# Kernel optimization log

Measured on AMD Instinct MI355X. Metric: run time of the kernel, lower is better.

## Reference

```python
import math
import jax, jax.numpy as jnp
import numpy as np

NQ = 10      # n_qubits
NB = 4       # n_blocks (angle encoding layers)
VD = 6       # vqc_depth (hardware-efficient layers)
LAT = 128    # latent_dim
NOBS = 9     # n_qubits - k_local + 1 sliding 2-local groups
DIM = 2 ** NQ


def sin_embed(t, dim):
    half = dim // 2
    freqs = jnp.exp(-math.log(10000.0) * jnp.arange(half, dtype=jnp.float32) / half)
    args = t[:, None] * freqs[None, :]
    return jnp.concatenate([jnp.cos(args), jnp.sin(args)], axis=-1)


def apply_ry(psi, theta, q):
    # psi: [B, 2^NQ] complex; theta: scalar or [B]
    B = psi.shape[0]
    p = psi.reshape(B, 2 ** q, 2, 2 ** (NQ - 1 - q))
    th = jnp.broadcast_to(theta, (B,))
    c = jnp.cos(th / 2)[:, None, None].astype(psi.dtype)
    s = jnp.sin(th / 2)[:, None, None].astype(psi.dtype)
    p0, p1 = p[:, :, 0, :], p[:, :, 1, :]
    return jnp.stack([c * p0 - s * p1, s * p0 + c * p1], axis=2).reshape(B, -1)


def apply_cnot(psi, ctrl, tgt):
    B = psi.shape[0]
    pt = psi.reshape((B,) + (2,) * NQ)
    p0 = jax.lax.index_in_dim(pt, 0, axis=ctrl + 1, keepdims=True)
    p1 = jnp.flip(jax.lax.index_in_dim(pt, 1, axis=ctrl + 1, keepdims=True), axis=tgt + 1)
    return jnp.concatenate([p0, p1], axis=ctrl + 1).reshape(B, -1)


def run_circuit(enc, var_params):
    B = enc.shape[0]
    psi = jnp.zeros((B, DIM), dtype=jnp.complex64).at[:, 0].set(1.0)
    # angle encoding: RY data re-uploading blocks with CNOT ladders between blocks
    for layer in range(NB):
        for q in range(NQ):
            psi = apply_ry(psi, enc[:, layer * NQ + q], q)
        if layer < NB - 1:
            for q in range(0, NQ - 1, 2):
                psi = apply_cnot(psi, q, q + 1)
            for q in range(1, NQ - 1, 2):
                psi = apply_cnot(psi, q, q + 1)
    # hardware-efficient variational layers
    for ly in range(VD):
        for q in range(NQ):
            psi = apply_ry(psi, var_params[ly, q], q)
        for q in range(0, NQ - 1, 2):
            psi = apply_cnot(psi, q, q + 1)
        for q in range(1, NQ - 1, 2):
            psi = apply_cnot(psi, q, q + 1)
    return psi


def build_H(A_p, B_p, D_p):
    # create_Hermitian: lower-tri (row-major) = A + iB; h[i-1,i-1] = D[i]; H = h + h^dagger
    r, c = np.tril_indices(4, -1)  # order matches count+j loop: (1,0),(2,0),(2,1),(3,0),(3,1),(3,2)
    L = jnp.zeros((NOBS, 4, 4), dtype=jnp.complex64)
    L = L.at[:, r, c].set(A_p.astype(jnp.complex64) + 1j * B_p.astype(jnp.complex64))
    d = 2.0 * jnp.concatenate([D_p[:, 1:4], jnp.zeros((NOBS, 1), dtype=D_p.dtype)], axis=1)
    H = L + jnp.conj(jnp.swapaxes(L, 1, 2))
    H = H + jax.vmap(jnp.diag)(d).astype(jnp.complex64)
    return H


def expvals(psi, H):
    B = psi.shape[0]
    outs = []
    for s in range(NOBS):  # sliding window [s, s+1]
        pg = psi.reshape(B, 2 ** s, 4, 2 ** (NQ - s - 2))
        outs.append(jnp.einsum('balr,lk,bakr->b', jnp.conj(pg), H[s], pg).real)
    return jnp.stack(outs, axis=-1)


def setup_inputs() -> dict:
    ks = jax.random.split(jax.random.key(0), 12)
    B = 2048
    return {
        'z_t': jax.random.normal(ks[0], (B, LAT), dtype=jnp.float32),
        't': jax.random.uniform(ks[1], (B,), dtype=jnp.float32),
        'W1': 0.05 * jax.random.normal(ks[2], (2 * LAT, 256), dtype=jnp.float32),
        'b1': jnp.zeros((256,), dtype=jnp.float32),
        'W2': 0.05 * jax.random.normal(ks[3], (256, NB * NQ), dtype=jnp.float32),
        'b2': jnp.zeros((NB * NQ,), dtype=jnp.float32),
        'var_params': 0.01 * jax.random.normal(ks[4], (VD, NQ), dtype=jnp.float32),
        'A_p': 2.0 * jax.random.normal(ks[5], (NOBS, 6), dtype=jnp.float32),
        'B_p': 2.0 * jax.random.normal(ks[6], (NOBS, 6), dtype=jnp.float32),
        'D_p': 2.0 * jax.random.normal(ks[7], (NOBS, 4), dtype=jnp.float32),
        'W3': 0.05 * jax.random.normal(ks[8], (NOBS, 256), dtype=jnp.float32),
        'b3': jnp.zeros((256,), dtype=jnp.float32),
        'W4': 0.05 * jax.random.normal(ks[9], (256, LAT), dtype=jnp.float32),
        'b4': jnp.zeros((LAT,), dtype=jnp.float32),
    }


def reference(z_t, t, W1, b1, W2, b2, var_params, A_p, B_p, D_p, W3, b3, W4, b4):
    x = jnp.concatenate([z_t, sin_embed(t, LAT)], axis=-1)   # [B, 2*LAT]
    h = jax.nn.silu(x @ W1 + b1)
    enc = h @ W2 + b2                                         # [B, NB*NQ]
    psi = run_circuit(enc, var_params)                        # [B, 2^NQ]
    obs = expvals(psi, build_H(A_p, B_p, D_p))                # [B, NOBS]
    return jax.nn.silu(obs @ W3 + b3) @ W4 + b4               # [B, LAT]
```

## Files before the change

### kernel.cpp

```cpp
#include <hip/hip_runtime.h>
#include <math.h>

#define NOBS 9
#define LATD 128

typedef unsigned u32x2 __attribute__((ext_vector_type(2)));

__device__ __forceinline__ float silu_f(float x) { return x / (1.f + expf(-x)); }


template<int CTRL>
__device__ __forceinline__ float dpp_perm(float x) {
  return __int_as_float(__builtin_amdgcn_update_dpp(0, __float_as_int(x), CTRL, 0xF, 0xF, true));
}
template<int PAT>
__device__ __forceinline__ float ds_swz(float x) {
  return __int_as_float(__builtin_amdgcn_ds_swizzle(__float_as_int(x), PAT));
}

__device__ __forceinline__ float x4(float x) { return ds_swz<0x101F>(x); }

#if __has_builtin(__builtin_amdgcn_permlane32_swap)
#define PL32 1
__device__ __forceinline__ float x32(float x, bool sel) {
  u32x2 r = __builtin_amdgcn_permlane32_swap(__float_as_uint(x), __float_as_uint(x), false, false);
  return __uint_as_float(sel ? r.x : r.y);
}
__device__ __forceinline__ float sum32(float x) {
  u32x2 r = __builtin_amdgcn_permlane32_swap(__float_as_uint(x), __float_as_uint(x), false, false);
  return __uint_as_float(r.x) + __uint_as_float(r.y);
}
#else
#define PL32 0
__device__ __forceinline__ float x32(float x, bool sel) { return __shfl_xor(x, 32, 64); }
__device__ __forceinline__ float sum32(float x) { return x + __shfl_xor(x, 32, 64); }
#endif

#if __has_builtin(__builtin_amdgcn_permlane16_swap)
#define PL16 1
__device__ __forceinline__ float x16(float x, bool sel) {
  u32x2 r = __builtin_amdgcn_permlane16_swap(__float_as_uint(x), __float_as_uint(x), false, false);
  return __uint_as_float(sel ? r.x : r.y);
}
__device__ __forceinline__ float sum16(float x) {
  u32x2 r = __builtin_amdgcn_permlane16_swap(__float_as_uint(x), __float_as_uint(x), false, false);
  return __uint_as_float(r.x) + __uint_as_float(r.y);
}
#else
#define PL16 0
__device__ __forceinline__ float x16(float x, bool sel) { return ds_swz<0x401F>(x); }
__device__ __forceinline__ float sum16(float x) { return x + ds_swz<0x401F>(x); }
#endif

__device__ __forceinline__ float wave_sum(float x) {
  x += dpp_perm<0xB1>(x);
  x += dpp_perm<0x4E>(x);
  x += x4(x);
  x += dpp_perm<0x128>(x);
  x = sum16(x);
  x = sum32(x);
  return x;
}


template<int M>
__device__ __forceinline__ void ry_reg(float v[16], float c, float s) {
#pragma unroll
  for (int r = 0; r < 16; ++r) {
    if ((r & M) == 0) {
      float p0 = v[r], p1 = v[r | M];
      v[r]     = c * p0 - s * p1;
      v[r | M] = s * p0 + c * p1;
    }
  }
}

__device__ __forceinline__ void apply_rys(float v[16], int lane, bool sel32, bool sel16,
                                          const float* __restrict__ cc,
                                          const float* __restrict__ ss) {
  ry_reg<8>(v, cc[0], ss[0]);
  ry_reg<4>(v, cc[1], ss[1]);
  ry_reg<2>(v, cc[2], ss[2]);
  ry_reg<1>(v, cc[3], ss[3]);
  { float c = cc[4], s = ss[4], sp = (lane & 32) ? s : -s;
#pragma unroll
    for (int r = 0; r < 16; ++r) { float p = x32(v[r], sel32); v[r] = fmaf(c, v[r], sp * p); } }
  { float c = cc[5], s = ss[5], sp = (lane & 16) ? s : -s;
#pragma unroll
    for (int r = 0; r < 16; ++r) { float p = x16(v[r], sel16); v[r] = fmaf(c, v[r], sp * p); } }
  { float c = cc[6], s = ss[6], sp = (lane & 8) ? s : -s;
#pragma unroll
    for (int r = 0; r < 16; ++r) { float p = dpp_perm<0x128>(v[r]); v[r] = fmaf(c, v[r], sp * p); } }
  { float c = cc[7], s = ss[7], sp = (lane & 4) ? s : -s;
#pragma unroll
    for (int r = 0; r < 16; ++r) { float p = x4(v[r]); v[r] = fmaf(c, v[r], sp * p); } }
  { float c = cc[8], s = ss[8], sp = (lane & 2) ? s : -s;
#pragma unroll
    for (int r = 0; r < 16; ++r) { float p = dpp_perm<0x4E>(v[r]); v[r] = fmaf(c, v[r], sp * p); } }
  { float c = cc[9], s = ss[9], sp = (lane & 1) ? s : -s;
#pragma unroll
    for (int r = 0; r < 16; ++r) { float p = dpp_perm<0xB1>(v[r]); v[r] = fmaf(c, v[r], sp * p); } }
}

__device__ __forceinline__ void cnot_ladder(float v[16], int lane, bool sel32, bool sel16) {
  float t;
  t=v[8];  v[8]=v[12];  v[12]=t;
  t=v[9];  v[9]=v[13];  v[13]=t;
  t=v[10]; v[10]=v[14]; v[14]=t;
  t=v[11]; v[11]=v[15]; v[15]=t;
  t=v[2];  v[2]=v[3];   v[3]=t;
  t=v[6];  v[6]=v[7];   v[7]=t;
  t=v[10]; v[10]=v[11]; v[11]=t;
  t=v[14]; v[14]=v[15]; v[15]=t;
  { bool c45 = (lane & 32);
#pragma unroll
    for (int r = 0; r < 16; ++r) { float p = x16(v[r], sel16); v[r] = c45 ? p : v[r]; } }
  { bool c67 = (lane & 8);
#pragma unroll
    for (int r = 0; r < 16; ++r) { float p = x4(v[r]); v[r] = c67 ? p : v[r]; } }
  { bool c89 = (lane & 2);
#pragma unroll
    for (int r = 0; r < 16; ++r) { float p = dpp_perm<0xB1>(v[r]); v[r] = c89 ? p : v[r]; } }
  t=v[4];  v[4]=v[6];   v[6]=t;
  t=v[5];  v[5]=v[7];   v[7]=t;
  t=v[12]; v[12]=v[14]; v[14]=t;
  t=v[13]; v[13]=v[15]; v[15]=t;
#pragma unroll
  for (int r = 1; r < 16; r += 2) v[r] = x32(v[r], sel32);
  { bool c56 = (lane & 16);
#pragma unroll
    for (int r = 0; r < 16; ++r) { float p = dpp_perm<0x128>(v[r]); v[r] = c56 ? p : v[r]; } }
  { bool c78 = (lane & 4);
#pragma unroll
    for (int r = 0; r < 16; ++r) { float p = dpp_perm<0x4E>(v[r]); v[r] = c78 ? p : v[r]; } }
}


__global__ __launch_bounds__(256) void fused_kernel(
    const float* __restrict__ z, const float* __restrict__ t,
    const float* __restrict__ W1, const float* __restrict__ b1,
    const float* __restrict__ W2, const float* __restrict__ b2,
    const float* __restrict__ varp,
    const float* __restrict__ A_p, const float* __restrict__ D_p,
    const float* __restrict__ W3, const float* __restrict__ b3,
    const float* __restrict__ W4, const float* __restrict__ b4,
    float* __restrict__ out) {
  __shared__ float xs[4][256];
  __shared__ float hs[4][256];
  __shared__ float dump[4][1024];
  __shared__ float cs[4][40], sn[4][40];
  __shared__ float vcs[60], vsn[60];
  __shared__ float os[4][NOBS];

  int tid = threadIdx.x;
  int b0 = blockIdx.x * 4;

  if (tid < 60) {
    float s, c;
    sincosf(0.5f * varp[tid], &s, &c);
    vcs[tid] = c; vsn[tid] = s;
  }

#pragma unroll
  for (int r = 0; r < 4; ++r) {
    int b = b0 + r;
    if (tid < 128) {
      xs[r][tid] = z[b * 128 + tid];
    } else {
      int i = tid - 128, j = i & 63;
      float freq = expf(-9.2103403719761836f * (float)j * (1.f / 64.f));
      float arg = t[b] * freq;
      xs[r][tid] = (i < 64) ? cosf(arg) : sinf(arg);
    }
  }
  __syncthreads();

  {
    float bv = b1[tid];
    float a0 = bv, a1 = bv, a2 = bv, a3 = bv;
#pragma unroll 4
    for (int k = 0; k < 256; k += 4) {
      float w0 = W1[(k + 0) * 256 + tid];
      float w1 = W1[(k + 1) * 256 + tid];
      float w2 = W1[(k + 2) * 256 + tid];
      float w3 = W1[(k + 3) * 256 + tid];
      float4 x0 = *(const float4*)&xs[0][k];
      float4 x1 = *(const float4*)&xs[1][k];
      float4 x2 = *(const float4*)&xs[2][k];
      float4 x3 = *(const float4*)&xs[3][k];
      a0 = fmaf(x0.w, w3, fmaf(x0.z, w2, fmaf(x0.y, w1, fmaf(x0.x, w0, a0))));
      a1 = fmaf(x1.w, w3, fmaf(x1.z, w2, fmaf(x1.y, w1, fmaf(x1.x, w0, a1))));
      a2 = fmaf(x2.w, w3, fmaf(x2.z, w2, fmaf(x2.y, w1, fmaf(x2.x, w0, a2))));
      a3 = fmaf(x3.w, w3, fmaf(x3.z, w2, fmaf(x3.y, w1, fmaf(x3.x, w0, a3))));
    }
    hs[0][tid] = silu_f(a0);
    hs[1][tid] = silu_f(a1);
    hs[2][tid] = silu_f(a2);
    hs[3][tid] = silu_f(a3);
  }
  __syncthreads();

  if (tid < 160) {
    int r = tid / 40, c = tid - r * 40;
    float acc = b2[c];
#pragma unroll 4
    for (int k = 0; k < 256; k += 4) {
      float4 h = *(const float4*)&hs[r][k];
      acc = fmaf(h.x, W2[(k + 0) * 40 + c], acc);
      acc = fmaf(h.y, W2[(k + 1) * 40 + c], acc);
      acc = fmaf(h.z, W2[(k + 2) * 40 + c], acc);
      acc = fmaf(h.w, W2[(k + 3) * 40 + c], acc);
    }
    float s, cv;
    sincosf(0.5f * acc, &s, &cv);
    cs[r][c] = cv; sn[r][c] = s;
  }
  __syncthreads();

  {
    int wave = tid >> 6;
    int lane = tid & 63;
    bool sel32 = true, sel16 = true;
#if PL32
    { u32x2 tt = __builtin_amdgcn_permlane32_swap((unsigned)lane, (unsigned)lane, false, false);
      sel32 = (tt.x == (unsigned)(lane ^ 32)); }
#endif
#if PL16
    { u32x2 tt = __builtin_amdgcn_permlane16_swap((unsigned)lane, (unsigned)lane, false, false);
      sel16 = (tt.x == (unsigned)(lane ^ 16)); }
#endif
    const float* cc = cs[wave];
    const float* ss = sn[wave];

    float base = 1.f;
    base *= (lane & 32) ? ss[4] : cc[4];
    base *= (lane & 16) ? ss[5] : cc[5];
    base *= (lane & 8)  ? ss[6] : cc[6];
    base *= (lane & 4)  ? ss[7] : cc[7];
    base *= (lane & 2)  ? ss[8] : cc[8];
    base *= (lane & 1)  ? ss[9] : cc[9];
    float v[16];
#pragma unroll
    for (int r = 0; r < 16; ++r) {
      float p = base;
      p *= (r & 8) ? ss[0] : cc[0];
      p *= (r & 4) ? ss[1] : cc[1];
      p *= (r & 2) ? ss[2] : cc[2];
      p *= (r & 1) ? ss[3] : cc[3];
      v[r] = p;
    }
    cnot_ladder(v, lane, sel32, sel16);
#pragma unroll 1
    for (int layer = 1; layer < 4; ++layer) {
      apply_rys(v, lane, sel32, sel16, cc + layer * 10, ss + layer * 10);
      if (layer < 3) cnot_ladder(v, lane, sel32, sel16);
    }
#pragma unroll 1
    for (int ly = 0; ly < 6; ++ly) {
      apply_rys(v, lane, sel32, sel16, vcs + ly * 10, vsn + ly * 10);
      cnot_ladder(v, lane, sel32, sel16);
    }

    float* sw = dump[wave];
#pragma unroll
    for (int r = 0; r < 16; ++r) sw[r * 64 + lane] = v[r];

#pragma unroll 1
    for (int s = 0; s < NOBS; ++s) {
      const int r8 = 8 - s;
      const int stride = 1 << r8;
      float h10 = A_p[s*6+0], h20 = A_p[s*6+1], h21 = A_p[s*6+2];
      float h30 = A_p[s*6+3], h31 = A_p[s*6+4], h32 = A_p[s*6+5];
      float d0 = 2.f * D_p[s*4+1], d1 = 2.f * D_p[s*4+2], d2 = 2.f * D_p[s*4+3];
      float acc = 0.f;
#pragma unroll
      for (int k = 0; k < 4; ++k) {
        int p = lane + 64 * k;
        int a  = p >> r8;
        int rr = p & (stride - 1);
        int bse = (a << (r8 + 2)) + rr;
        float x0 = sw[bse];
        float x1 = sw[bse + stride];
        float x2 = sw[bse + 2 * stride];
        float x3 = sw[bse + 3 * stride];
        acc += d0 * x0 * x0 + d1 * x1 * x1 + d2 * x2 * x2
             + 2.f * (h10 * x1 * x0 + h20 * x2 * x0 + h21 * x2 * x1
                    + h30 * x3 * x0 + h31 * x3 * x1 + h32 * x3 * x2);
      }
      acc = wave_sum(acc);
      if (lane == 0) os[wave][s] = acc;
    }
  }
  __syncthreads();

  {
    float bv = b3[tid];
    float a0 = bv, a1 = bv, a2 = bv, a3 = bv;
#pragma unroll
    for (int s = 0; s < NOBS; ++s) {
      float w = W3[s * 256 + tid];
      a0 = fmaf(os[0][s], w, a0);
      a1 = fmaf(os[1][s], w, a1);
      a2 = fmaf(os[2][s], w, a2);
      a3 = fmaf(os[3][s], w, a3);
    }
    hs[0][tid] = silu_f(a0);
    hs[1][tid] = silu_f(a1);
    hs[2][tid] = silu_f(a2);
    hs[3][tid] = silu_f(a3);
  }
  __syncthreads();
  {
    int c = tid & 127, rg = tid >> 7;
    const float* h0 = hs[rg * 2];
    const float* h1 = hs[rg * 2 + 1];
    float o0 = b4[c], o1 = b4[c];
#pragma unroll 4
    for (int k = 0; k < 256; k += 4) {
      float w0 = W4[(k + 0) * 128 + c];
      float w1 = W4[(k + 1) * 128 + c];
      float w2 = W4[(k + 2) * 128 + c];
      float w3 = W4[(k + 3) * 128 + c];
      float4 ha = *(const float4*)&h0[k];
      float4 hb = *(const float4*)&h1[k];
      o0 = fmaf(ha.w, w3, fmaf(ha.z, w2, fmaf(ha.y, w1, fmaf(ha.x, w0, o0))));
      o1 = fmaf(hb.w, w3, fmaf(hb.z, w2, fmaf(hb.y, w1, fmaf(hb.x, w0, o1))));
    }
    out[(b0 + rg * 2) * LATD + c]     = o0;
    out[(b0 + rg * 2 + 1) * LATD + c] = o1;
  }
}


extern "C" void kernel_launch(void* const* d_in, const int* in_sizes, int n_in,
                              void* d_out, int out_size, void* d_ws, size_t ws_size,
                              hipStream_t stream) {
  const float* z_t  = (const float*)d_in[0];
  const float* t    = (const float*)d_in[1];
  const float* W1   = (const float*)d_in[2];
  const float* b1   = (const float*)d_in[3];
  const float* W2   = (const float*)d_in[4];
  const float* b2   = (const float*)d_in[5];
  const float* varp = (const float*)d_in[6];
  const float* A_p  = (const float*)d_in[7];
  const float* D_p  = (const float*)d_in[9];
  const float* W3   = (const float*)d_in[10];
  const float* b3   = (const float*)d_in[11];
  const float* W4   = (const float*)d_in[12];
  const float* b4   = (const float*)d_in[13];
  float* out = (float*)d_out;

  int B = in_sizes[1];

  fused_kernel<<<B / 4, 256, 0, stream>>>(z_t, t, W1, b1, W2, b2, varp,
                                          A_p, D_p, W3, b3, W4, b4, out);
}
```

Baseline: 128.8 us.

## Split each statevector across two waves with LDS exchange for top qubit

Each batch row's 1024-amplitude state is now split across two wavefronts (8 registers each instead of 16), with the most significant qubit's RY handled by exchanging halves through shared memory under a block barrier. Blocks now process 2 rows instead of 4, doubling the grid, and the permlane swap intrinsics are replaced with plain shfl_xor. The intent is more parallelism and lower register pressure per wave. The cost is a __syncthreads per RY layer, double the W1/W4 weight traffic per row, and slower shuffle-based cross-lane ops.

Measured after the change: 128.2 us. Within noise of the previous version (-0.5%).

```diff
diff --git a/kernel.cpp b/kernel.cpp
--- a/kernel.cpp
+++ b/kernel.cpp
@@ -3,8 +3,6 @@
 
 #define NOBS 9
 #define LATD 128
-
-typedef unsigned u32x2 __attribute__((ext_vector_type(2)));
 
 __device__ __forceinline__ float silu_f(float x) { return x / (1.f + expf(-x)); }
 
@@ -17,56 +15,23 @@
 __device__ __forceinline__ float ds_swz(float x) {
   return __int_as_float(__builtin_amdgcn_ds_swizzle(__float_as_int(x), PAT));
 }
-
-__device__ __forceinline__ float x4(float x) { return ds_swz<0x101F>(x); }
-
-#if __has_builtin(__builtin_amdgcn_permlane32_swap)
-#define PL32 1
-__device__ __forceinline__ float x32(float x, bool sel) {
-  u32x2 r = __builtin_amdgcn_permlane32_swap(__float_as_uint(x), __float_as_uint(x), false, false);
-  return __uint_as_float(sel ? r.x : r.y);
-}
-__device__ __forceinline__ float sum32(float x) {
-  u32x2 r = __builtin_amdgcn_permlane32_swap(__float_as_uint(x), __float_as_uint(x), false, false);
-  return __uint_as_float(r.x) + __uint_as_float(r.y);
-}
-#else
-#define PL32 0
-__device__ __forceinline__ float x32(float x, bool sel) { return __shfl_xor(x, 32, 64); }
-__device__ __forceinline__ float sum32(float x) { return x + __shfl_xor(x, 32, 64); }
-#endif
-
-#if __has_builtin(__builtin_amdgcn_permlane16_swap)
-#define PL16 1
-__device__ __forceinline__ float x16(float x, bool sel) {
-  u32x2 r = __builtin_amdgcn_permlane16_swap(__float_as_uint(x), __float_as_uint(x), false, false);
-  return __uint_as_float(sel ? r.x : r.y);
-}
-__device__ __forceinline__ float sum16(float x) {
-  u32x2 r = __builtin_amdgcn_permlane16_swap(__float_as_uint(x), __float_as_uint(x), false, false);
-  return __uint_as_float(r.x) + __uint_as_float(r.y);
-}
-#else
-#define PL16 0
-__device__ __forceinline__ float x16(float x, bool sel) { return ds_swz<0x401F>(x); }
-__device__ __forceinline__ float sum16(float x) { return x + ds_swz<0x401F>(x); }
-#endif
+__device__ __forceinline__ float x4f(float x) { return ds_swz<0x101F>(x); }
 
 __device__ __forceinline__ float wave_sum(float x) {
   x += dpp_perm<0xB1>(x);
   x += dpp_perm<0x4E>(x);
-  x += x4(x);
+  x += x4f(x);
   x += dpp_perm<0x128>(x);
-  x = sum16(x);
-  x = sum32(x);
+  x += ds_swz<0x401F>(x);
+  x += __shfl_xor(x, 32, 64);
   return x;
 }
 
 
 template<int M>
-__device__ __forceinline__ void ry_reg(float v[16], float c, float s) {
-#pragma unroll
-  for (int r = 0; r < 16; ++r) {
+__device__ __forceinline__ void ry_reg8(float v[8], float c, float s) {
+#pragma unroll
+  for (int r = 0; r < 8; ++r) {
     if ((r & M) == 0) {
       float p0 = v[r], p1 = v[r | M];
       v[r]     = c * p0 - s * p1;
@@ -74,65 +39,78 @@
     }
   }
 }
-
-__device__ __forceinline__ void apply_rys(float v[16], int lane, bool sel32, bool sel16,
-                                          const float* __restrict__ cc,
-                                          const float* __restrict__ ss) {
-  ry_reg<8>(v, cc[0], ss[0]);
-  ry_reg<4>(v, cc[1], ss[1]);
-  ry_reg<2>(v, cc[2], ss[2]);
-  ry_reg<1>(v, cc[3], ss[3]);
-  { float c = cc[4], s = ss[4], sp = (lane & 32) ? s : -s;
-#pragma unroll
-    for (int r = 0; r < 16; ++r) { float p = x32(v[r], sel32); v[r] = fmaf(c, v[r], sp * p); } }
-  { float c = cc[5], s = ss[5], sp = (lane & 16) ? s : -s;
-#pragma unroll
-    for (int r = 0; r < 16; ++r) { float p = x16(v[r], sel16); v[r] = fmaf(c, v[r], sp * p); } }
-  { float c = cc[6], s = ss[6], sp = (lane & 8) ? s : -s;
-#pragma unroll
-    for (int r = 0; r < 16; ++r) { float p = dpp_perm<0x128>(v[r]); v[r] = fmaf(c, v[r], sp * p); } }
-  { float c = cc[7], s = ss[7], sp = (lane & 4) ? s : -s;
-#pragma unroll
-    for (int r = 0; r < 16; ++r) { float p = x4(v[r]); v[r] = fmaf(c, v[r], sp * p); } }
-  { float c = cc[8], s = ss[8], sp = (lane & 2) ? s : -s;
-#pragma unroll
-    for (int r = 0; r < 16; ++r) { float p = dpp_perm<0x4E>(v[r]); v[r] = fmaf(c, v[r], sp * p); } }
-  { float c = cc[9], s = ss[9], sp = (lane & 1) ? s : -s;
-#pragma unroll
-    for (int r = 0; r < 16; ++r) { float p = dpp_perm<0xB1>(v[r]); v[r] = fmaf(c, v[r], sp * p); } }
-}
-
-__device__ __forceinline__ void cnot_ladder(float v[16], int lane, bool sel32, bool sel16) {
-  float t;
-  t=v[8];  v[8]=v[12];  v[12]=t;
-  t=v[9];  v[9]=v[13];  v[13]=t;
-  t=v[10]; v[10]=v[14]; v[14]=t;
-  t=v[11]; v[11]=v[15]; v[15]=t;
-  t=v[2];  v[2]=v[3];   v[3]=t;
-  t=v[6];  v[6]=v[7];   v[7]=t;
-  t=v[10]; v[10]=v[11]; v[11]=t;
-  t=v[14]; v[14]=v[15]; v[15]=t;
+template<int MASK>
+__device__ __forceinline__ void ry_shfl8(float v[8], float c, float s, int lane) {
+  float sp = (lane & MASK) ? s : -s;
+#pragma unroll
+  for (int r = 0; r < 8; ++r) { float p = __shfl_xor(v[r], MASK, 64); v[r] = fmaf(c, v[r], sp * p); }
+}
+template<int CTRL, int MASK>
+__device__ __forceinline__ void ry_dpp8(float v[8], float c, float s, int lane) {
+  float sp = (lane & MASK) ? s : -s;
+#pragma unroll
+  for (int r = 0; r < 8; ++r) { float p = dpp_perm<CTRL>(v[r]); v[r] = fmaf(c, v[r], sp * p); }
+}
+__device__ __forceinline__ void ry_x4g(float v[8], float c, float s, int lane) {
+  float sp = (lane & 4) ? s : -s;
+#pragma unroll
+  for (int r = 0; r < 8; ++r) { float p = x4f(v[r]); v[r] = fmaf(c, v[r], sp * p); }
+}
+
+__device__ __forceinline__ void apply_rys10(float v[8], int lane, int w,
+                                            const float* __restrict__ cc,
+                                            const float* __restrict__ ss,
+                                            float* xbuf) {
+  {
+    float c = cc[0], s = ss[0];
+    float sp = w ? s : -s;
+    float* mine   = xbuf + w * 512;
+    float* theirs = xbuf + (1 - w) * 512;
+#pragma unroll
+    for (int r = 0; r < 8; ++r) mine[r * 64 + lane] = v[r];
+    __syncthreads();
+#pragma unroll
+    for (int r = 0; r < 8; ++r) { float p = theirs[r * 64 + lane]; v[r] = fmaf(c, v[r], sp * p); }
+  }
+  ry_reg8<4>(v, cc[1], ss[1]);
+  ry_reg8<2>(v, cc[2], ss[2]);
+  ry_reg8<1>(v, cc[3], ss[3]);
+  ry_shfl8<32>(v, cc[4], ss[4], lane);
+  ry_shfl8<16>(v, cc[5], ss[5], lane);
+  ry_dpp8<0x128, 8>(v, cc[6], ss[6], lane);
+  ry_x4g(v, cc[7], ss[7], lane);
+  ry_dpp8<0x4E, 2>(v, cc[8], ss[8], lane);
+  ry_dpp8<0xB1, 1>(v, cc[9], ss[9], lane);
+}
+
+__device__ __forceinline__ void cnot_ladder8(float v[8], int lane, int w) {
+#pragma unroll
+  for (int r = 0; r < 4; ++r) {
+    float a = v[r], b = v[r + 4];
+    v[r]     = w ? b : a;
+    v[r + 4] = w ? a : b;
+  }
+  { float t = v[2]; v[2] = v[3]; v[3] = t; }
+  { float t = v[6]; v[6] = v[7]; v[7] = t; }
   { bool c45 = (lane & 32);
 #pragma unroll
-    for (int r = 0; r < 16; ++r) { float p = x16(v[r], sel16); v[r] = c45 ? p : v[r]; } }
+    for (int r = 0; r < 8; ++r) { float p = __shfl_xor(v[r], 16, 64); v[r] = c45 ? p : v[r]; } }
   { bool c67 = (lane & 8);
 #pragma unroll
-    for (int r = 0; r < 16; ++r) { float p = x4(v[r]); v[r] = c67 ? p : v[r]; } }
+    for (int r = 0; r < 8; ++r) { float p = x4f(v[r]); v[r] = c67 ? p : v[r]; } }
   { bool c89 = (lane & 2);
 #pragma unroll
-    for (int r = 0; r < 16; ++r) { float p = dpp_perm<0xB1>(v[r]); v[r] = c89 ? p : v[r]; } }
-  t=v[4];  v[4]=v[6];   v[6]=t;
-  t=v[5];  v[5]=v[7];   v[7]=t;
-  t=v[12]; v[12]=v[14]; v[14]=t;
-  t=v[13]; v[13]=v[15]; v[15]=t;
-#pragma unroll
-  for (int r = 1; r < 16; r += 2) v[r] = x32(v[r], sel32);
+    for (int r = 0; r < 8; ++r) { float p = dpp_perm<0xB1>(v[r]); v[r] = c89 ? p : v[r]; } }
+  { float t = v[4]; v[4] = v[6]; v[6] = t; }
+  { float t = v[5]; v[5] = v[7]; v[7] = t; }
+#pragma unroll
+  for (int r = 1; r < 8; r += 2) v[r] = __shfl_xor(v[r], 32, 64);
   { bool c56 = (lane & 16);
 #pragma unroll
-    for (int r = 0; r < 16; ++r) { float p = dpp_perm<0x128>(v[r]); v[r] = c56 ? p : v[r]; } }
+    for (int r = 0; r < 8; ++r) { float p = dpp_perm<0x128>(v[r]); v[r] = c56 ? p : v[r]; } }
   { bool c78 = (lane & 4);
 #pragma unroll
-    for (int r = 0; r < 16; ++r) { float p = dpp_perm<0x4E>(v[r]); v[r] = c78 ? p : v[r]; } }
+    for (int r = 0; r < 8; ++r) { float p = dpp_perm<0x4E>(v[r]); v[r] = c78 ? p : v[r]; } }
 }
 
 
@@ -145,15 +123,16 @@
     const float* __restrict__ W3, const float* __restrict__ b3,
     const float* __restrict__ W4, const float* __restrict__ b4,
     float* __restrict__ out) {
-  __shared__ float xs[4][256];
-  __shared__ float hs[4][256];
-  __shared__ float dump[4][1024];
-  __shared__ float cs[4][40], sn[4][40];
+  __shared__ float xs[2][256];
+  __shared__ float hs[2][256];
+  __shared__ float xch[2][2][1024];
+  __shared__ float cs[2][40], sn[2][40];
   __shared__ float vcs[60], vsn[60];
-  __shared__ float os[4][NOBS];
+  __shared__ float part[2][2][NOBS];
+  __shared__ float os[2][NOBS];
 
   int tid = threadIdx.x;
-  int b0 = blockIdx.x * 4;
+  int b0 = blockIdx.x * 2;
 
   if (tid < 60) {
     float s, c;
@@ -162,7 +141,7 @@
   }
 
 #pragma unroll
-  for (int r = 0; r < 4; ++r) {
+  for (int r = 0; r < 2; ++r) {
     int b = b0 + r;
     if (tid < 128) {
       xs[r][tid] = z[b * 128 + tid];
@@ -176,8 +155,7 @@
   __syncthreads();
 
   {
-    float bv = b1[tid];
-    float a0 = bv, a1 = bv, a2 = bv, a3 = bv;
+    float a0 = b1[tid], a1 = a0;
 #pragma unroll 4
     for (int k = 0; k < 256; k += 4) {
       float w0 = W1[(k + 0) * 256 + tid];
@@ -186,21 +164,15 @@
       float w3 = W1[(k + 3) * 256 + tid];
       float4 x0 = *(const float4*)&xs[0][k];
       float4 x1 = *(const float4*)&xs[1][k];
-      float4 x2 = *(const float4*)&xs[2][k];
-      float4 x3 = *(const float4*)&xs[3][k];
       a0 = fmaf(x0.w, w3, fmaf(x0.z, w2, fmaf(x0.y, w1, fmaf(x0.x, w0, a0))));
       a1 = fmaf(x1.w, w3, fmaf(x1.z, w2, fmaf(x1.y, w1, fmaf(x1.x, w0, a1))));
-      a2 = fmaf(x2.w, w3, fmaf(x2.z, w2, fmaf(x2.y, w1, fmaf(x2.x, w0, a2))));
-      a3 = fmaf(x3.w, w3, fmaf(x3.z, w2, fmaf(x3.y, w1, fmaf(x3.x, w0, a3))));
     }
     hs[0][tid] = silu_f(a0);
     hs[1][tid] = silu_f(a1);
-    hs[2][tid] = silu_f(a2);
-    hs[3][tid] = silu_f(a3);
-  }
-  __syncthreads();
-
-  if (tid < 160) {
+  }
+  __syncthreads();
+
+  if (tid < 80) {
     int r = tid / 40, c = tid - r * 40;
     float acc = b2[c];
 #pragma unroll 4
@@ -217,54 +189,57 @@
   }
   __syncthreads();
 
-  {
-    int wave = tid >> 6;
-    int lane = tid & 63;
-    bool sel32 = true, sel16 = true;
-#if PL32
-    { u32x2 tt = __builtin_amdgcn_permlane32_swap((unsigned)lane, (unsigned)lane, false, false);
-      sel32 = (tt.x == (unsigned)(lane ^ 32)); }
-#endif
-#if PL16
-    { u32x2 tt = __builtin_amdgcn_permlane16_swap((unsigned)lane, (unsigned)lane, false, false);
-      sel16 = (tt.x == (unsigned)(lane ^ 16)); }
-#endif
-    const float* cc = cs[wave];
-    const float* ss = sn[wave];
-
-    float base = 1.f;
+  float v[8];
+  int W_id = tid >> 6;
+  int row  = W_id >> 1;
+  int w    = W_id & 1;
+  int lane = tid & 63;
+  const float* cc = cs[row];
+  const float* ss = sn[row];
+  float* xch_row = &xch[row][0][0];
+
+  {
+    float base = w ? ss[0] : cc[0];
     base *= (lane & 32) ? ss[4] : cc[4];
     base *= (lane & 16) ? ss[5] : cc[5];
     base *= (lane & 8)  ? ss[6] : cc[6];
     base *= (lane & 4)  ? ss[7] : cc[7];
     base *= (lane & 2)  ? ss[8] : cc[8];
     base *= (lane & 1)  ? ss[9] : cc[9];
-    float v[16];
-#pragma unroll
-    for (int r = 0; r < 16; ++r) {
+#pragma unroll
+    for (int r = 0; r < 8; ++r) {
       float p = base;
-      p *= (r & 8) ? ss[0] : cc[0];
       p *= (r & 4) ? ss[1] : cc[1];
       p *= (r & 2) ? ss[2] : cc[2];
       p *= (r & 1) ? ss[3] : cc[3];
       v[r] = p;
     }
-    cnot_ladder(v, lane, sel32, sel16);
+  }
+  cnot_ladder8(v, lane, w);
+  int idx = 0;
 #pragma unroll 1
-    for (int layer = 1; layer < 4; ++layer) {
-      apply_rys(v, lane, sel32, sel16, cc + layer * 10, ss + layer * 10);
-      if (layer < 3) cnot_ladder(v, lane, sel32, sel16);
-    }
+  for (int layer = 1; layer < 4; ++layer) {
+    apply_rys10(v, lane, w, cc + layer * 10, ss + layer * 10, xch_row + (idx & 1) * 1024);
+    ++idx;
+    if (layer < 3) cnot_ladder8(v, lane, w);
+  }
 #pragma unroll 1
-    for (int ly = 0; ly < 6; ++ly) {
-      apply_rys(v, lane, sel32, sel16, vcs + ly * 10, vsn + ly * 10);
-      cnot_ladder(v, lane, sel32, sel16);
-    }
-
-    float* sw = dump[wave];
-#pragma unroll
-    for (int r = 0; r < 16; ++r) sw[r * 64 + lane] = v[r];
-
+  for (int ly = 0; ly < 6; ++ly) {
+    apply_rys10(v, lane, w, vcs + ly * 10, vsn + ly * 10, xch_row + (idx & 1) * 1024);
+    ++idx;
+    cnot_ladder8(v, lane, w);
+  }
+
+  {
+    float* dmp = xch_row + 1024;
+#pragma unroll
+    for (int r = 0; r < 8; ++r) dmp[w * 512 + r * 64 + lane] = v[r];
+  }
+  __syncthreads();
+
+  {
+    const float* dmp = xch_row + 1024;
+    int wl = w * 64 + lane;
 #pragma unroll 1
     for (int s = 0; s < NOBS; ++s) {
       const int r8 = 8 - s;
@@ -274,60 +249,56 @@
       float d0 = 2.f * D_p[s*4+1], d1 = 2.f * D_p[s*4+2], d2 = 2.f * D_p[s*4+3];
       float acc = 0.f;
 #pragma unroll
-      for (int k = 0; k < 4; ++k) {
-        int p = lane + 64 * k;
+      for (int k = 0; k < 2; ++k) {
+        int p = wl + 128 * k;
         int a  = p >> r8;
         int rr = p & (stride - 1);
         int bse = (a << (r8 + 2)) + rr;
-        float x0 = sw[bse];
-        float x1 = sw[bse + stride];
-        float x2 = sw[bse + 2 * stride];
-        float x3 = sw[bse + 3 * stride];
+        float x0 = dmp[bse];
+        float x1 = dmp[bse + stride];
+        float x2 = dmp[bse + 2 * stride];
+        float x3 = dmp[bse + 3 * stride];
         acc += d0 * x0 * x0 + d1 * x1 * x1 + d2 * x2 * x2
              + 2.f * (h10 * x1 * x0 + h20 * x2 * x0 + h21 * x2 * x1
                     + h30 * x3 * x0 + h31 * x3 * x1 + h32 * x3 * x2);
       }
       acc = wave_sum(acc);
-      if (lane == 0) os[wave][s] = acc;
-    }
-  }
-  __syncthreads();
-
-  {
-    float bv = b3[tid];
-    float a0 = bv, a1 = bv, a2 = bv, a3 = bv;
+      if (lane == 0) part[row][w][s] = acc;
+    }
+  }
+  __syncthreads();
+  if (tid < 2 * NOBS) {
+    int r = tid / NOBS, s = tid - r * NOBS;
+    os[r][s] = part[r][0][s] + part[r][1][s];
+  }
+  __syncthreads();
+
+  {
+    float a0 = b3[tid], a1 = a0;
 #pragma unroll
     for (int s = 0; s < NOBS; ++s) {
-      float w = W3[s * 256 + tid];
-      a0 = fmaf(os[0][s], w, a0);
-      a1 = fmaf(os[1][s], w, a1);
-      a2 = fmaf(os[2][s], w, a2);
-      a3 = fmaf(os[3][s], w, a3);
+      float wv = W3[s * 256 + tid];
+      a0 = fmaf(os[0][s], wv, a0);
+      a1 = fmaf(os[1][s], wv, a1);
     }
     hs[0][tid] = silu_f(a0);
     hs[1][tid] = silu_f(a1);
-    hs[2][tid] = silu_f(a2);
-    hs[3][tid] = silu_f(a3);
   }
   __syncthreads();
   {
     int c = tid & 127, rg = tid >> 7;
-    const float* h0 = hs[rg * 2];
-    const float* h1 = hs[rg * 2 + 1];
-    float o0 = b4[c], o1 = b4[c];
+    const float* h = hs[rg];
+    float o = b4[c];
 #pragma unroll 4
     for (int k = 0; k < 256; k += 4) {
       float w0 = W4[(k + 0) * 128 + c];
       float w1 = W4[(k + 1) * 128 + c];
       float w2 = W4[(k + 2) * 128 + c];
       float w3 = W4[(k + 3) * 128 + c];
-      float4 ha = *(const float4*)&h0[k];
-      float4 hb = *(const float4*)&h1[k];
-      o0 = fmaf(ha.w, w3, fmaf(ha.z, w2, fmaf(ha.y, w1, fmaf(ha.x, w0, o0))));
-      o1 = fmaf(hb.w, w3, fmaf(hb.z, w2, fmaf(hb.y, w1, fmaf(hb.x, w0, o1))));
-    }
-    out[(b0 + rg * 2) * LATD + c]     = o0;
-    out[(b0 + rg * 2 + 1) * LATD + c] = o1;
+      float4 ha = *(const float4*)&h[k];
+      o = fmaf(ha.w, w3, fmaf(ha.z, w2, fmaf(ha.y, w1, fmaf(ha.x, w0, o))));
+    }
+    out[(b0 + rg) * LATD + c] = o;
   }
 }
 
@@ -352,6 +323,6 @@
 
   int B = in_sizes[1];
 
-  fused_kernel<<<B / 4, 256, 0, stream>>>(z_t, t, W1, b1, W2, b2, varp,
+  fused_kernel<<<B / 2, 256, 0, stream>>>(z_t, t, W1, b1, W2, b2, varp,
                                           A_p, D_p, W3, b3, W4, b4, out);
 }
```
